# Performance work log

Measured on AMD Instinct MI355X. Metric: run time of the kernel, lower is better.

## Reference

```python
import jax, jax.numpy as jnp
import numpy as np
import math

B, S, D, H, HD, P = 2, 2048, 2048, 16, 128, 10
ROPE_BASE = 10000.0


def _rope_tables(seq_len, head_dim):
    inv_freq = 1.0 / (ROPE_BASE ** (np.arange(0, head_dim, 2, dtype=np.float32) / head_dim))
    t = np.arange(seq_len, dtype=np.float32)
    freqs = np.outer(t, inv_freq)                  # [S, hd/2]
    emb = np.concatenate([freqs, freqs], axis=-1)  # [S, hd]
    return jnp.asarray(np.cos(emb)), jnp.asarray(np.sin(emb))


def _rotate_half(x):
    half = x.shape[-1] // 2
    return jnp.concatenate([-x[..., half:], x[..., :half]], axis=-1)


def setup_inputs() -> dict:
    key = jax.random.key(0)
    ks = jax.random.split(key, 8)
    hidden_states = jax.random.normal(ks[0], (B, S, D), dtype=jnp.float32)
    # causal additive mask, llama convention: 0 where allowed, large negative above diagonal
    causal = jnp.triu(jnp.full((S, S), -1e9, dtype=jnp.float32), k=1)
    attention_mask = jnp.broadcast_to(causal[None, None], (B, 1, S, S))
    position_ids = jnp.broadcast_to(jnp.arange(S, dtype=jnp.int64)[None], (B, S))
    scale = 1.0 / math.sqrt(D)
    Wq = jax.random.normal(ks[1], (D, D), dtype=jnp.float32) * scale
    Wk = jax.random.normal(ks[2], (D, D), dtype=jnp.float32) * scale
    Wv = jax.random.normal(ks[3], (D, D), dtype=jnp.float32) * scale
    Wo = jax.random.normal(ks[4], (D, D), dtype=jnp.float32) * scale
    adapter_query = jax.random.normal(ks[5], (P, D), dtype=jnp.float32)
    adapter_gate = jax.random.normal(ks[6], (1, H, 1, 1), dtype=jnp.float32) * 0.1
    return dict(hidden_states=hidden_states, attention_mask=attention_mask,
                position_ids=position_ids, Wq=Wq, Wk=Wk, Wv=Wv, Wo=Wo,
                adapter_query=adapter_query, adapter_gate=adapter_gate)


def reference(hidden_states, attention_mask, position_ids, Wq, Wk, Wv, Wo,
              adapter_query, adapter_gate):
    bsz, q_len, _ = hidden_states.shape
    inv_sqrt_hd = 1.0 / math.sqrt(HD)

    def split_heads(x):  # [B,S,D] -> [B,H,S,hd]
        return x.reshape(bsz, q_len, H, HD).transpose(0, 2, 1, 3)

    q = split_heads(hidden_states @ Wq)
    k = split_heads(hidden_states @ Wk)
    v = split_heads(hidden_states @ Wv)

    # RoPE
    cos_t, sin_t = _rope_tables(q_len, HD)
    cos = cos_t[position_ids][:, None]  # [B,1,S,hd]
    sin = sin_t[position_ids][:, None]
    q = q * cos + _rotate_half(q) * sin
    k = k * cos + _rotate_half(k) * sin

    # main attention
    scores = jnp.einsum('bhqd,bhkd->bhqk', q, k) * inv_sqrt_hd
    scores = scores + attention_mask
    attn = jax.nn.softmax(scores.astype(jnp.float32), axis=-1).astype(q.dtype)
    attn_out = jnp.einsum('bhqk,bhkd->bhqd', attn, v)

    # adapter: soft prompt projected through k/v proj (learn_kv=False), no RoPE
    adapter = jnp.broadcast_to(adapter_query[None], (bsz, P, D))  # [B,P,D]
    a_k = (adapter @ Wk).reshape(bsz, P, H, HD).transpose(0, 2, 1, 3)  # [B,H,P,hd]
    a_v = (adapter @ Wv).reshape(bsz, P, H, HD).transpose(0, 2, 1, 3)
    a_scores = jnp.einsum('bhqd,bhpd->bhqp', q, a_k) * inv_sqrt_hd
    a_w = adapter_gate * jax.nn.softmax(a_scores.astype(jnp.float32), axis=-1).astype(q.dtype)
    a_out = jnp.einsum('bhqp,bhpd->bhqd', a_w, a_v)

    out = attn_out + a_out
    out = out.transpose(0, 2, 1, 3).reshape(bsz, q_len, D)
    return out @ Wo
```

## Files before the change

### kernel.cpp

```cpp
#include <hip/hip_runtime.h>
#include <cstdint>
#include <cstddef>

typedef __bf16 bf16x8 __attribute__((ext_vector_type(8)));
typedef float  f32x4  __attribute__((ext_vector_type(4)));

__device__ __forceinline__ unsigned short f2bf(float f) {
  unsigned int u = __float_as_uint(f);
  u += 0x7FFF + ((u >> 16) & 1);
  return (unsigned short)(u >> 16);
}
__device__ __forceinline__ float bf2f(unsigned short u) {
  return __uint_as_float(((unsigned int)u) << 16);
}

#define SEQ 2048
#define DMODEL 2048
#define NH 16
#define HD 128
#define NB 2
#define NP 10
#define MAUG 4106
#define SCALEL2 (0.08838834764831845f * 1.44269504088896340f)

#define GLOAD_LDS16(g, l) \
  __builtin_amdgcn_global_load_lds((__attribute__((address_space(1))) const void*)(g), \
                                   (__attribute__((address_space(3))) void*)(l), 16, 0, 0)

#define FENCE() asm volatile("" ::: "memory")
#define SBAR() do { FENCE(); __builtin_amdgcn_s_barrier(); FENCE(); } while (0)
#define WAITVM(N) asm volatile("s_waitcnt vmcnt(" #N ")" ::: "memory")

__global__ void k_tables(float* __restrict__ cost, float* __restrict__ sint) {
  int idx = blockIdx.x * 256 + threadIdx.x;
  if (idx >= SEQ * 64) return;
  int s = idx >> 6, i = idx & 63;
  double invf = exp(-((double)(2 * i) / 128.0) * log(10000.0));
  double a = (double)s * invf;
  float c = (float)cos(a), sn = (float)sin(a);
  cost[s * HD + i] = c;  cost[s * HD + 64 + i] = c;
  sint[s * HD + i] = sn; sint[s * HD + 64 + i] = sn;
}

__global__ __launch_bounds__(256) void k_wt(const float* __restrict__ W0,
                                            const float* __restrict__ W1,
                                            const float* __restrict__ W2,
                                            const float* __restrict__ W3,
                                            unsigned short* __restrict__ out) {
  __shared__ float tile[32][33];
  const float* W = (blockIdx.z == 0) ? W0 : (blockIdx.z == 1) ? W1 : (blockIdx.z == 2) ? W2 : W3;
  unsigned short* o = out + (size_t)blockIdx.z * DMODEL * DMODEL;
  int bx = blockIdx.x * 32, by = blockIdx.y * 32;
  int tx = threadIdx.x & 31, ty = threadIdx.x >> 5;
  #pragma unroll
  for (int j = 0; j < 32; j += 8)
    tile[ty + j][tx] = W[(size_t)(bx + ty + j) * DMODEL + by + tx];
  __syncthreads();
  #pragma unroll
  for (int j = 0; j < 32; j += 8)
    o[(size_t)(by + ty + j) * DMODEL + bx + tx] = f2bf(tile[tx][ty + j]);
}

__global__ void k_xaug(const float* __restrict__ X, const float* __restrict__ Aq,
                       unsigned short* __restrict__ xaug) {
  size_t idx = (size_t)blockIdx.x * 256 + threadIdx.x;
  if (idx >= (size_t)MAUG * DMODEL) return;
  size_t row = idx >> 11;
  int col = (int)(idx & 2047);
  float v = (row < (size_t)NB * SEQ) ? X[idx] : Aq[(row - NB * SEQ) * DMODEL + col];
  xaug[idx] = f2bf(v);
}

#define RD_A(dst, bb, MH) do { \
  _Pragma("unroll") for (int i_ = 0; i_ < 4; i_++) \
    _Pragma("unroll") for (int ks_ = 0; ks_ < 2; ks_++) \
      dst[i_][ks_] = *(const bf16x8*)&lds[(bb) + (wr*128 + (MH)*64 + i_*16 + lr)*64 + (((ks_*4+quad) ^ (lr & 7)) * 8)]; \
} while (0)

#define RD_B(dst, bb, NHH) do { \
  _Pragma("unroll") for (int j_ = 0; j_ < 2; j_++) \
    _Pragma("unroll") for (int ks_ = 0; ks_ < 2; ks_++) \
      dst[j_][ks_] = *(const bf16x8*)&lds[(bb) + 16384 + (wc*64 + (NHH)*32 + j_*16 + lr)*64 + (((ks_*4+quad) ^ (lr & 7)) * 8)]; \
} while (0)

#define MM(A, B, MH, NHH) do { \
  __builtin_amdgcn_s_setprio(1); \
  _Pragma("unroll") for (int i_ = 0; i_ < 4; i_++) \
    _Pragma("unroll") for (int j_ = 0; j_ < 2; j_++) { \
      acc[(MH)*4+i_][(NHH)*2+j_] = __builtin_amdgcn_mfma_f32_16x16x32_bf16(A[i_][0], B[j_][0], acc[(MH)*4+i_][(NHH)*2+j_], 0, 0, 0); \
      acc[(MH)*4+i_][(NHH)*2+j_] = __builtin_amdgcn_mfma_f32_16x16x32_bf16(A[i_][1], B[j_][1], acc[(MH)*4+i_][(NHH)*2+j_], 0, 0, 0); \
    } \
  __builtin_amdgcn_s_setprio(0); \
} while (0)

#define STG_AE(nb, ko) do { \
  GLOAD_LDS16(sA + (ko),                      &lds[(nb)*32768 + (qrow)*64 + g8]); \
  GLOAD_LDS16(sA + 128*(size_t)DMODEL + (ko), &lds[(nb)*32768 + (128+qrow)*64 + g8]); } while (0)
#define STG_AO(nb, ko) do { \
  GLOAD_LDS16(sA + 64*(size_t)DMODEL + (ko),  &lds[(nb)*32768 + (64+qrow)*64 + g8]); \
  GLOAD_LDS16(sA + 192*(size_t)DMODEL + (ko), &lds[(nb)*32768 + (192+qrow)*64 + g8]); } while (0)
#define STG_BE(nb, ko) do { \
  GLOAD_LDS16(sB + (ko),                      &lds[(nb)*32768 + 16384 + (qb)*64 + g8]); \
  GLOAD_LDS16(sB + 128*(size_t)DMODEL + (ko), &lds[(nb)*32768 + 16384 + (128+qb)*64 + g8]); } while (0)
#define STG_BO(nb, ko) do { \
  GLOAD_LDS16(sB + 32*(size_t)DMODEL + (ko),  &lds[(nb)*32768 + 16384 + (32+qb)*64 + g8]); \
  GLOAD_LDS16(sB + 160*(size_t)DMODEL + (ko), &lds[(nb)*32768 + 16384 + (160+qb)*64 + g8]); } while (0)

template<int BF16OUT>
__global__ __launch_bounds__(512, 2) void k_gemm256(const unsigned short* __restrict__ A,
                                                    const unsigned short* __restrict__ Bt,
                                                    void* __restrict__ Cv,
                                                    int M, size_t c_stride_mat) {
  __shared__ unsigned short lds[65536];
  const int t = threadIdx.x;
  const int lane = t & 63, w = t >> 6;
  const int lr = lane & 15, quad = lane >> 4;
  const int wr = w >> 2, wc = w & 3;
  const int tm = (M + 255) >> 8;
  const int perz = tm * 8;
  const int qchunk = gridDim.x >> 3;
  const int lin = ((int)blockIdx.x & 7) * qchunk + ((int)blockIdx.x >> 3);
  const int z = lin / perz;
  const int rem = lin - z * perz;
  const int m0 = (rem >> 3) * 256, n0 = (rem & 7) * 256;
  const unsigned short* Bz = Bt + (size_t)z * DMODEL * DMODEL;

  const int qrow = t >> 3;
  const int g8 = (t & 7) * 8;
  const int gsw8 = (((t & 7) ^ (qrow & 7)) * 8);
  const int qb = (qrow < 32) ? qrow : qrow + 32;

  const unsigned short* sA = A + (size_t)(m0 + qrow) * DMODEL + gsw8;
  const unsigned short* sB = Bz + (size_t)(n0 + qb) * DMODEL + gsw8;

  bf16x8 aE[4][2], aO[4][2], bE[2][2], bO[2][2];
  f32x4 acc[8][4];
  #pragma unroll
  for (int i = 0; i < 8; i++)
    #pragma unroll
    for (int j = 0; j < 4; j++) acc[i][j] = (f32x4){0.f, 0.f, 0.f, 0.f};

  STG_AE(0, 0); STG_BE(0, 0); STG_BO(0, 0); STG_AO(0, 0);
  WAITVM(4);
  SBAR();
  RD_A(aE, 0, 0); RD_B(bE, 0, 0);

  for (int kt = 0; kt < DMODEL / 64; kt++) {
    const int base = (kt & 1) << 15;
    const int nb2 = (kt & 1) ^ 1;
    const int nbase = nb2 << 15;
    const int ko = (kt + 1) * 64;
    const bool more = (kt + 1 < DMODEL / 64);

    if (more) { STG_AE(nb2, ko); WAITVM(4); } else WAITVM(2);
    SBAR();
    RD_B(bO, base, 1);
    MM(aE, bE, 0, 0);

    if (more) { STG_BE(nb2, ko); WAITVM(4); } else WAITVM(0);
    SBAR();
    RD_A(aO, base, 1);
    MM(aE, bO, 0, 1);

    if (more) STG_BO(nb2, ko);
    MM(aO, bE, 1, 0);

    if (more) {
      STG_AO(nb2, ko);
      WAITVM(4);
      SBAR();
      RD_A(aE, nbase, 0); RD_B(bE, nbase, 0);
    }
    MM(aO, bO, 1, 1);
  }

  #pragma unroll
  for (int mi = 0; mi < 8; mi++) {
    #pragma unroll
    for (int r = 0; r < 4; r++) {
      int row = m0 + wr * 128 + mi * 16 + quad * 4 + r;
      if (row < M) {
        if (BF16OUT) {
          unsigned short* C = (unsigned short*)Cv + (size_t)z * c_stride_mat;
          #pragma unroll
          for (int n = 0; n < 4; n++)
            C[(size_t)row * DMODEL + n0 + wc * 64 + n * 16 + lr] = f2bf(acc[mi][n][r]);
        } else {
          float* C = (float*)Cv + (size_t)z * c_stride_mat;
          #pragma unroll
          for (int n = 0; n < 4; n++)
            C[(size_t)row * DMODEL + n0 + wc * 64 + n * 16 + lr] = acc[mi][n][r];
        }
      }
    }
  }
}

#define O_LDA(MH) do { \
  _Pragma("unroll") for (int i_ = 0; i_ < 2; i_++) \
    _Pragma("unroll") for (int ks_ = 0; ks_ < 2; ks_++) \
      a[i_][ks_] = *(const bf16x8*)&lds[base + (wr*64 + ((MH)*2+i_)*16 + lr)*64 + (((ks_*4+quad) ^ (lr & 7)) * 8)]; \
} while (0)

#define O_LDB(NHH) do { \
  _Pragma("unroll") for (int j_ = 0; j_ < 2; j_++) \
    _Pragma("unroll") for (int ks_ = 0; ks_ < 2; ks_++) \
      b[(NHH)*2+j_][ks_] = *(const bf16x8*)&lds[base + 8192 + (wc*64 + ((NHH)*2+j_)*16 + lr)*64 + (((ks_*4+quad) ^ (lr & 7)) * 8)]; \
} while (0)

#define O_MFMA(MH, NHH) do { \
  __builtin_amdgcn_s_setprio(1); \
  _Pragma("unroll") for (int i_ = 0; i_ < 2; i_++) \
    _Pragma("unroll") for (int j_ = 0; j_ < 2; j_++) { \
      acc[(MH)*2+i_][(NHH)*2+j_] = __builtin_amdgcn_mfma_f32_16x16x32_bf16(a[i_][0], b[(NHH)*2+j_][0], acc[(MH)*2+i_][(NHH)*2+j_], 0, 0, 0); \
      acc[(MH)*2+i_][(NHH)*2+j_] = __builtin_amdgcn_mfma_f32_16x16x32_bf16(a[i_][1], b[(NHH)*2+j_][1], acc[(MH)*2+i_][(NHH)*2+j_], 0, 0, 0); \
    } \
  __builtin_amdgcn_s_setprio(0); \
} while (0)

#define O_STG_AE(nb, ko) GLOAD_LDS16(sA + (ko), &lds[(nb)*24576 + (qb)*64 + g8])
#define O_STG_AO(nb, ko) GLOAD_LDS16(sA + 32*(size_t)DMODEL + (ko), &lds[(nb)*24576 + (32+qb)*64 + g8])
#define O_STG_BE(nb, ko) do { \
  GLOAD_LDS16(sB + (ko),                      &lds[(nb)*24576 + 8192 + (qb)*64 + g8]); \
  GLOAD_LDS16(sB + 128*(size_t)DMODEL + (ko), &lds[(nb)*24576 + 8192 + (128+qb)*64 + g8]); } while (0)
#define O_STG_BO(nb, ko) do { \
  GLOAD_LDS16(sB + 32*(size_t)DMODEL + (ko),  &lds[(nb)*24576 + 8192 + (32+qb)*64 + g8]); \
  GLOAD_LDS16(sB + 160*(size_t)DMODEL + (ko), &lds[(nb)*24576 + 8192 + (160+qb)*64 + g8]); } while (0)

__global__ __launch_bounds__(512, 2) void k_gemmo(const unsigned short* __restrict__ A,
                                                  const unsigned short* __restrict__ Bt,
                                                  float* __restrict__ C) {
  __shared__ unsigned short lds[49152];
  const int t = threadIdx.x;
  const int lane = t & 63, w = t >> 6;
  const int lr = lane & 15, quad = lane >> 4;
  const int wr = w >> 2, wc = w & 3;
  const int lin = ((int)blockIdx.x & 7) * 32 + ((int)blockIdx.x >> 3);
  const int m0 = (lin >> 3) * 128, n0 = (lin & 7) * 256;

  const int qrow = t >> 3;
  const int g8 = (t & 7) * 8;
  const int gsw8 = (((t & 7) ^ (qrow & 7)) * 8);
  const int qb = (qrow < 32) ? qrow : qrow + 32;

  const unsigned short* sA = A + (size_t)(m0 + qb) * DMODEL + gsw8;
  const unsigned short* sB = Bt + (size_t)(n0 + qb) * DMODEL + gsw8;

  bf16x8 a[2][2], b[4][2];
  f32x4 acc[4][4];
  #pragma unroll
  for (int i = 0; i < 4; i++)
    #pragma unroll
    for (int j = 0; j < 4; j++) acc[i][j] = (f32x4){0.f, 0.f, 0.f, 0.f};

  O_STG_AE(0, 0); O_STG_BE(0, 0); O_STG_BO(0, 0); O_STG_AO(0, 0);
  WAITVM(3);
  SBAR();

  for (int kt = 0; kt < DMODEL / 64; kt++) {
    const int base = (kt & 1) * 24576;
    const int nb = (kt & 1) ^ 1;
    const int ko = (kt + 1) * 64;
    const bool more = (kt + 1 < DMODEL / 64);

    O_LDA(0);
    O_LDB(0);
    if (more) O_STG_AE(nb, ko);
    SBAR();
    O_MFMA(0, 0);
    if (more) WAITVM(2); else WAITVM(1);
    SBAR();

    O_LDB(1);
    if (more) O_STG_BE(nb, ko);
    SBAR();
    O_MFMA(0, 1);
    if (more) WAITVM(3); else WAITVM(0);
    SBAR();

    O_LDA(1);
    if (more) O_STG_BO(nb, ko);
    SBAR();
    O_MFMA(1, 0);
    SBAR();

    if (more) O_STG_AO(nb, ko);
    SBAR();
    O_MFMA(1, 1);
    if (more) WAITVM(3);
    SBAR();
  }

  #pragma unroll
  for (int mi = 0; mi < 4; mi++) {
    #pragma unroll
    for (int r = 0; r < 4; r++) {
      int row = m0 + wr * 64 + mi * 16 + quad * 4 + r;
      #pragma unroll
      for (int n = 0; n < 4; n++)
        C[(size_t)row * DMODEL + n0 + wc * 64 + n * 16 + lr] = acc[mi][n][r];
    }
  }
}

__global__ __launch_bounds__(256) void k_rope(const unsigned short* __restrict__ Qf,
                                              const unsigned short* __restrict__ Kf,
                                              const unsigned short* __restrict__ Vf,
                                              const float* __restrict__ cost, const float* __restrict__ sint,
                                              unsigned short* __restrict__ Qb, unsigned short* __restrict__ Kb,
                                              unsigned short* __restrict__ AKb, unsigned short* __restrict__ avt) {
  int row = blockIdx.x;
  int t = threadIdx.x;
  int c0 = t * 8;
  size_t off = (size_t)row * DMODEL + c0;
  if (row < NB * SEQ) {
    int s = row & (SEQ - 1);
    int d0 = c0 & (HD - 1);
    int po = (d0 < 64) ? 64 : -64;
    float sign = (d0 < 64) ? -1.f : 1.f;
    uint4 qv = *(const uint4*)&Qf[off];
    uint4 qp = *(const uint4*)&Qf[off + po];
    uint4 kv = *(const uint4*)&Kf[off];
    uint4 kp = *(const uint4*)&Kf[off + po];
    const unsigned short* qa = (const unsigned short*)&qv;
    const unsigned short* qb2 = (const unsigned short*)&qp;
    const unsigned short* ka = (const unsigned short*)&kv;
    const unsigned short* kb2 = (const unsigned short*)&kp;
    unsigned short oq[8], ok[8];
    #pragma unroll
    for (int j = 0; j < 8; j++) {
      float cv = cost[s * HD + d0 + j], sv = sint[s * HD + d0 + j];
      oq[j] = f2bf(bf2f(qa[j]) * cv + sign * bf2f(qb2[j]) * sv);
      ok[j] = f2bf(bf2f(ka[j]) * cv + sign * bf2f(kb2[j]) * sv);
    }
    *(uint4*)&Qb[off] = *(const uint4*)oq;
    *(uint4*)&Kb[off] = *(const uint4*)ok;
  } else {
    int p = row - NB * SEQ;
    uint4 kv = *(const uint4*)&Kf[off];
    uint4 vv = *(const uint4*)&Vf[off];
    *(uint4*)&AKb[(size_t)p * DMODEL + c0] = kv;
    const unsigned short* vp = (const unsigned short*)&vv;
    #pragma unroll
    for (int j = 0; j < 8; j++)
      avt[(size_t)(c0 + j) * 32 + p] = vp[j];
    if (p == 0) {
      #pragma unroll
      for (int j = 0; j < 8; j++)
        for (int pp = NP; pp < 32; pp++)
          avt[(size_t)(c0 + j) * 32 + pp] = 0;
    }
  }
}

__global__ __launch_bounds__(256) void k_vt(const unsigned short* __restrict__ Vf,
                                            unsigned short* __restrict__ Vt) {
  __shared__ unsigned short tile[64][72];
  const int t = threadIdx.x;
  int s0 = blockIdx.x * 64;
  int d0 = blockIdx.y * 64;
  int b = blockIdx.z >> 4, h = blockIdx.z & 15;
  #pragma unroll
  for (int j = t; j < 512; j += 256) {
    int row = j >> 3, ch = j & 7;
    *(uint4*)&tile[row][ch * 8] =
      *(const uint4*)&Vf[(size_t)(b * SEQ + s0 + row) * DMODEL + h * HD + d0 + ch * 8];
  }
  __syncthreads();
  #pragma unroll
  for (int j = t; j < 512; j += 256) {
    int dr = j >> 3, ch = j & 7;
    unsigned short tmp[8];
    #pragma unroll
    for (int k = 0; k < 8; k++) tmp[k] = tile[ch * 8 + k][dr];
    *(uint4*)&Vt[((size_t)((b * NH + h) * HD + d0 + dr)) * SEQ + s0 + ch * 8] = *(const uint4*)tmp;
  }
}

#define PSTR 68

__global__ __launch_bounds__(256, 2) void k_flash(const unsigned short* __restrict__ Qb,
                                               const unsigned short* __restrict__ Kb,
                                               const unsigned short* __restrict__ Vt,
                                               const unsigned short* __restrict__ AKb,
                                               const unsigned short* __restrict__ avt,
                                               const float* __restrict__ gate,
                                               unsigned short* __restrict__ Obuf,
                                               float* __restrict__ ml,
                                               unsigned short* __restrict__ Aout) {
  const int L = blockIdx.x;
  const int h = L & 15;
  const int slot = 39 - (L >> 4);
  const int b = blockIdx.y;
  int qt, j, P;
  if (slot < 4)       { qt = slot;               j = 0;          P = 1; }
  else if (slot < 12) { int s = slot - 4;  qt = 4 + (s >> 1);  j = s & 1; P = 2; }
  else if (slot < 24) { int s = slot - 12; qt = 8 + s / 3;     j = s % 3; P = 3; }
  else                { int s = slot - 24; qt = 12 + (s >> 2); j = s & 3; P = 4; }

  const int t = threadIdx.x, w = t >> 6, lane = t & 63;
  const int lr = lane & 15, quad = lane >> 4;

  __shared__ unsigned short Ks[64 * 128];
  __shared__ unsigned short Vs[128 * 64];
  __shared__ unsigned short Ps[4][32 * PSTR];
  unsigned short* Ps16 = &Ps[w][0];

  const int row_base = qt * 128 + w * 32;

  bf16x8 qf[2][4];
  #pragma unroll
  for (int mt = 0; mt < 2; mt++)
    #pragma unroll
    for (int kk = 0; kk < 4; kk++)
      qf[mt][kk] = *(const bf16x8*)&Qb[((size_t)(b * SEQ + row_base + mt * 16 + lr)) * DMODEL
                                       + h * HD + kk * 32 + quad * 8];

  f32x4 o[2][8];
  #pragma unroll
  for (int mt = 0; mt < 2; mt++)
    #pragma unroll
    for (int nt = 0; nt < 8; nt++) o[mt][nt] = (f32x4){0.f, 0.f, 0.f, 0.f};
  float l_i[2][4];
  #pragma unroll
  for (int mt = 0; mt < 2; mt++)
    #pragma unroll
    for (int r = 0; r < 4; r++) l_i[mt][r] = 0.f;

  const int krow = t >> 4;
  const int vd = t >> 3, vc = (t & 7) ^ (vd & 7);
  const int ktend = 2 * qt + 2;

  for (int kt = j; kt < ktend; kt += P) {
    __syncthreads();
    #pragma unroll
    for (int jj = 0; jj < 4; jj++) {
      int row = krow + jj * 16;
      int c = (t & 15) ^ (row & 15);
      GLOAD_LDS16(&Kb[((size_t)(b * SEQ + kt * 64 + row)) * DMODEL + h * HD + c * 8],
                  &Ks[(t + jj * 256) * 8]);
    }
    #pragma unroll
    for (int jj = 0; jj < 4; jj++) {
      int d = vd + jj * 32;
      GLOAD_LDS16(&Vt[((size_t)((b * NH + h) * HD + d)) * SEQ + kt * 64 + vc * 8],
                  &Vs[(t + jj * 256) * 8]);
    }
    __syncthreads();

    f32x4 s4[2][4];
    #pragma unroll
    for (int mt = 0; mt < 2; mt++)
      #pragma unroll
      for (int nt = 0; nt < 4; nt++) s4[mt][nt] = (f32x4){0.f, 0.f, 0.f, 0.f};
    #pragma unroll
    for (int nt = 0; nt < 4; nt++)
      #pragma unroll
      for (int kk = 0; kk < 4; kk++) {
        bf16x8 bv = *(const bf16x8*)&Ks[((nt * 16 + lr) * 16 + ((kk * 4 + quad) ^ lr)) * 8];
        s4[0][nt] = __builtin_amdgcn_mfma_f32_16x16x32_bf16(qf[0][kk], bv, s4[0][nt], 0, 0, 0);
        s4[1][nt] = __builtin_amdgcn_mfma_f32_16x16x32_bf16(qf[1][kk], bv, s4[1][nt], 0, 0, 0);
      }

    const int maybe_mask = (kt * 64 + 63 > row_base);
    #pragma unroll
    for (int mt = 0; mt < 2; mt++) {
      #pragma unroll
      for (int nt = 0; nt < 4; nt++) s4[mt][nt] = s4[mt][nt] * SCALEL2;
      if (maybe_mask) {
        #pragma unroll
        for (int nt = 0; nt < 4; nt++) {
          int col = kt * 64 + nt * 16 + lr;
          #pragma unroll
          for (int r = 0; r < 4; r++)
            if (col > row_base + mt * 16 + quad * 4 + r) s4[mt][nt][r] = -__builtin_inff();
        }
      }
      #pragma unroll
      for (int nt = 0; nt < 4; nt++)
        #pragma unroll
        for (int r = 0; r < 4; r++) {
          float p = __builtin_amdgcn_exp2f(s4[mt][nt][r]);
          l_i[mt][r] += p;
          Ps[w][(mt * 16 + quad * 4 + r) * PSTR + nt * 16 + lr] = f2bf(p);
        }
    }
    #pragma unroll
    for (int kk2 = 0; kk2 < 2; kk2++) {
      bf16x8 af0 = *(const bf16x8*)&Ps[w][(lr) * PSTR + kk2 * 32 + quad * 8];
      bf16x8 af1 = *(const bf16x8*)&Ps[w][(16 + lr) * PSTR + kk2 * 32 + quad * 8];
      #pragma unroll
      for (int nt = 0; nt < 8; nt++) {
        bf16x8 bv = *(const bf16x8*)&Vs[((nt * 16 + lr) * 8 + ((kk2 * 4 + quad) ^ (lr & 7))) * 8];
        o[0][nt] = __builtin_amdgcn_mfma_f32_16x16x32_bf16(af0, bv, o[0][nt], 0, 0, 0);
        o[1][nt] = __builtin_amdgcn_mfma_f32_16x16x32_bf16(af1, bv, o[1][nt], 0, 0, 0);
      }
    }
  }

  #pragma unroll
  for (int mt = 0; mt < 2; mt++)
    #pragma unroll
    for (int r = 0; r < 4; r++) {
      float l = l_i[mt][r];
      #pragma unroll
      for (int off = 1; off < 16; off <<= 1) l += __shfl_xor(l, off, 64);
      l_i[mt][r] = l;
    }

  const size_t slotg = (size_t)(b * 16 + h) * 40 + slot;

  if (j == 0) {
    const float g = gate[h];
    #pragma unroll
    for (int mt = 0; mt < 2; mt++) {
      f32x4 as4 = (f32x4){0.f, 0.f, 0.f, 0.f};
      #pragma unroll
      for (int kk = 0; kk < 4; kk++) {
        bf16x8 akf = *(const bf16x8*)&AKb[(size_t)lr * DMODEL + h * HD + kk * 32 + quad * 8];
        as4 = __builtin_amdgcn_mfma_f32_16x16x32_bf16(qf[mt][kk], akf, as4, 0, 0, 0);
      }
      as4 = as4 * SCALEL2;
      float al[4];
      #pragma unroll
      for (int r = 0; r < 4; r++) {
        float p = (lr < NP) ? __builtin_amdgcn_exp2f(as4[r]) : 0.f;
        as4[r] = p;
        float sum = p;
        #pragma unroll
        for (int off = 1; off < 16; off <<= 1) sum += __shfl_xor(sum, off, 64);
        al[r] = sum;
      }
      #pragma unroll
      for (int r = 0; r < 4; r++) {
        Ps[w][(mt * 16 + quad * 4 + r) * PSTR + lr] = f2bf(as4[r]);
        Ps[w][(mt * 16 + quad * 4 + r) * PSTR + 16 + lr] = 0;
      }
      bf16x8 af = *(const bf16x8*)&Ps[w][(mt * 16 + lr) * PSTR + quad * 8];
      f32x4 pa[8];
      #pragma unroll
      for (int nt = 0; nt < 8; nt++) {
        bf16x8 bv = *(const bf16x8*)&avt[(size_t)(h * HD + nt * 16 + lr) * 32 + quad * 8];
        pa[nt] = __builtin_amdgcn_mfma_f32_16x16x32_bf16(af, bv, (f32x4){0.f, 0.f, 0.f, 0.f}, 0, 0, 0);
      }
      float invla[4];
      #pragma unroll
      for (int r = 0; r < 4; r++) invla[r] = g / al[r];
      #pragma unroll
      for (int nt = 0; nt < 8; nt++)
        #pragma unroll
        for (int r = 0; r < 4; r++)
          Ps16[(quad * 4 + r) * 128 + nt * 16 + lr] = f2bf(pa[nt][r] * invla[r]);
      size_t gb = (((size_t)(b * 16 + h) * 16 + qt)) * 16384 + (size_t)(w * 32 + mt * 16) * 128;
      #pragma unroll
      for (int it = 0; it < 4; it++) {
        int i = lane + it * 64;
        int rr = i >> 4, ch = i & 15;
        *(uint4*)&Aout[gb + rr * 128 + ch * 8] = *(const uint4*)&Ps16[rr * 128 + ch * 8];
      }
    }
  }

  #pragma unroll
  for (int mt = 0; mt < 2; mt++) {
    if (lr == 0) {
      #pragma unroll
      for (int r = 0; r < 4; r++) {
        int rl = w * 32 + mt * 16 + quad * 4 + r;
        ml[slotg * 128 + rl] = l_i[mt][r];
      }
    }
    #pragma unroll
    for (int nt = 0; nt < 8; nt++)
      #pragma unroll
      for (int r = 0; r < 4; r++)
        Ps16[(quad * 4 + r) * 128 + nt * 16 + lr] = f2bf(o[mt][nt][r]);
    size_t gb = slotg * 16384 + (size_t)(w * 32 + mt * 16) * 128;
    #pragma unroll
    for (int it = 0; it < 4; it++) {
      int i = lane + it * 64;
      int rr = i >> 4, ch = i & 15;
      *(uint4*)&Obuf[gb + rr * 128 + ch * 8] = *(const uint4*)&Ps16[rr * 128 + ch * 8];
    }
  }
}

__global__ __launch_bounds__(256) void k_merge(const unsigned short* __restrict__ Obuf,
                                               const float* __restrict__ ml,
                                               const unsigned short* __restrict__ Aout,
                                               unsigned short* __restrict__ ab) {
  int idx = blockIdx.x * 256 + threadIdx.x;
  int ch = idx & 15;
  int row = (idx >> 4) & 2047;
  int h = (idx >> 15) & 15;
  int b = idx >> 19;
  int qt = row >> 7, rl = row & 127;
  int start = qt < 4 ? qt : qt < 8 ? 4 + 2 * (qt - 4) : qt < 12 ? 12 + 3 * (qt - 8) : 24 + 4 * (qt - 12);
  int P = qt < 4 ? 1 : qt < 8 ? 2 : qt < 12 ? 3 : 4;
  size_t sbase = (size_t)(b * 16 + h) * 40 + start;
  float den = 0.f;
  float acc[8] = {0.f, 0.f, 0.f, 0.f, 0.f, 0.f, 0.f, 0.f};
  #pragma unroll
  for (int jp = 0; jp < 4; jp++) {
    if (jp < P) {
      den += ml[(sbase + jp) * 128 + rl];
      uint4 ov = *(const uint4*)&Obuf[(sbase + jp) * 16384 + rl * 128 + ch * 8];
      const unsigned short* pv = (const unsigned short*)&ov;
      #pragma unroll
      for (int k = 0; k < 8; k++) acc[k] += bf2f(pv[k]);
    }
  }
  uint4 av = *(const uint4*)&Aout[(((size_t)(b * 16 + h) * 16 + qt)) * 16384 + rl * 128 + ch * 8];
  const unsigned short* pa = (const unsigned short*)&av;
  float dn = 1.0f / den;
  unsigned short res[8];
  #pragma unroll
  for (int k = 0; k < 8; k++) res[k] = f2bf(acc[k] * dn + bf2f(pa[k]));
  *(uint4*)&ab[((size_t)(b * 2048 + row)) * 2048 + h * 128 + ch * 8] = *(const uint4*)res;
}

extern "C" void kernel_launch(void* const* d_in, const int* in_sizes, int n_in,
                              void* d_out, int out_size, void* d_ws, size_t ws_size,
                              hipStream_t stream) {
  const float* hidden = (const float*)d_in[0];
  const float* Wq = (const float*)d_in[3];
  const float* Wk = (const float*)d_in[4];
  const float* Wv = (const float*)d_in[5];
  const float* Wo = (const float*)d_in[6];
  const float* Aq = (const float*)d_in[7];
  const float* gate = (const float*)d_in[8];
  float* out = (float*)d_out;

  char* ws = (char*)d_ws;
  size_t off = 0;
  auto alloc = [&](size_t bytes) -> void* {
    void* p = ws + off;
    off = (off + bytes + 255) & ~(size_t)255;
    return p;
  };
  unsigned short* wt   = (unsigned short*)alloc((size_t)4 * DMODEL * DMODEL * 2);
  unsigned short* xaug = (unsigned short*)alloc((size_t)MAUG * DMODEL * 2);
  unsigned short* qkvb = (unsigned short*)alloc((size_t)3 * MAUG * DMODEL * 2);
  unsigned short* qf = qkvb;
  unsigned short* kf = qkvb + (size_t)MAUG * DMODEL;
  unsigned short* vf = kf + (size_t)MAUG * DMODEL;
  unsigned short* qb  = (unsigned short*)alloc((size_t)NB * SEQ * DMODEL * 2);
  unsigned short* kb  = (unsigned short*)alloc((size_t)NB * SEQ * DMODEL * 2);
  unsigned short* vt  = (unsigned short*)alloc((size_t)NB * SEQ * DMODEL * 2);
  unsigned short* akb = (unsigned short*)alloc((size_t)16 * DMODEL * 2);
  unsigned short* avt = (unsigned short*)alloc((size_t)DMODEL * 32 * 2);
  float* cost = (float*)alloc((size_t)SEQ * HD * 4);
  float* sint = (float*)alloc((size_t)SEQ * HD * 4);
  unsigned short* obuf = (unsigned short*)alloc((size_t)NB * NH * 40 * 16384 * 2);
  float* mlb = (float*)alloc((size_t)NB * NH * 40 * 128 * 4);
  unsigned short* aout = (unsigned short*)alloc((size_t)NB * NH * 16 * 16384 * 2);
  unsigned short* ab = qf;

  k_tables<<<SEQ * 64 / 256, 256, 0, stream>>>(cost, sint);
  k_wt<<<dim3(64, 64, 4), 256, 0, stream>>>(Wq, Wk, Wv, Wo, wt);
  {
    size_t n = (size_t)MAUG * DMODEL;
    k_xaug<<<(unsigned)((n + 255) / 256), 256, 0, stream>>>(hidden, Aq, xaug);
  }
  k_gemm256<1><<<dim3(408), 512, 0, stream>>>(xaug, wt, qkvb, MAUG, (size_t)MAUG * DMODEL);
  k_rope<<<MAUG, 256, 0, stream>>>(qf, kf, vf, cost, sint, qb, kb, akb, avt);
  k_vt<<<dim3(32, 2, 32), 256, 0, stream>>>(vf, vt);
  k_flash<<<dim3(640, 2), 256, 0, stream>>>(qb, kb, vt, akb, avt, gate, obuf, mlb, aout);
  k_merge<<<4096, 256, 0, stream>>>(obuf, mlb, aout, ab);
  k_gemmo<<<dim3(256), 512, 0, stream>>>(ab, wt + (size_t)3 * DMODEL * DMODEL, out);
}
```

Measured before the change: 420.1 us.

## Double-buffer K tiles and prefetch next K/V during attention compute

```diff
diff --git a/kernel.cpp b/kernel.cpp
--- a/kernel.cpp
+++ b/kernel.cpp
@@ -401,7 +401,7 @@
   const int t = threadIdx.x, w = t >> 6, lane = t & 63;
   const int lr = lane & 15, quad = lane >> 4;
 
-  __shared__ unsigned short Ks[64 * 128];
+  __shared__ unsigned short Ks[2 * 64 * 128];
   __shared__ unsigned short Vs[128 * 64];
   __shared__ unsigned short Ps[4][32 * PSTR];
   unsigned short* Ps16 = &Ps[w][0];
@@ -431,22 +431,28 @@
   const int vd = t >> 3, vc = (t & 7) ^ (vd & 7);
   const int ktend = 2 * qt + 2;
 
+  #pragma unroll
+  for (int jj = 0; jj < 4; jj++) {
+    int row = krow + jj * 16;
+    int c = (t & 15) ^ (row & 15);
+    GLOAD_LDS16(&Kb[((size_t)(b * SEQ + j * 64 + row)) * DMODEL + h * HD + c * 8],
+                &Ks[(t + jj * 256) * 8]);
+  }
+  #pragma unroll
+  for (int jj = 0; jj < 4; jj++) {
+    int d = vd + jj * 32;
+    GLOAD_LDS16(&Vt[((size_t)((b * NH + h) * HD + d)) * SEQ + j * 64 + vc * 8],
+                &Vs[(t + jj * 256) * 8]);
+  }
+
+  int kb = 0;
   for (int kt = j; kt < ktend; kt += P) {
-    __syncthreads();
-    #pragma unroll
-    for (int jj = 0; jj < 4; jj++) {
-      int row = krow + jj * 16;
-      int c = (t & 15) ^ (row & 15);
-      GLOAD_LDS16(&Kb[((size_t)(b * SEQ + kt * 64 + row)) * DMODEL + h * HD + c * 8],
-                  &Ks[(t + jj * 256) * 8]);
-    }
-    #pragma unroll
-    for (int jj = 0; jj < 4; jj++) {
-      int d = vd + jj * 32;
-      GLOAD_LDS16(&Vt[((size_t)((b * NH + h) * HD + d)) * SEQ + kt * 64 + vc * 8],
-                  &Vs[(t + jj * 256) * 8]);
-    }
-    __syncthreads();
+    const bool more = (kt + P < ktend);
+    const int kbase = kb * 8192;
+    const int nkbase = 8192 - kbase;
+
+    WAITVM(4);
+    SBAR();
 
     f32x4 s4[2][4];
     #pragma unroll
@@ -457,10 +463,20 @@
     for (int nt = 0; nt < 4; nt++)
       #pragma unroll
       for (int kk = 0; kk < 4; kk++) {
-        bf16x8 bv = *(const bf16x8*)&Ks[((nt * 16 + lr) * 16 + ((kk * 4 + quad) ^ lr)) * 8];
+        bf16x8 bv = *(const bf16x8*)&Ks[kbase + ((nt * 16 + lr) * 16 + ((kk * 4 + quad) ^ lr)) * 8];
         s4[0][nt] = __builtin_amdgcn_mfma_f32_16x16x32_bf16(qf[0][kk], bv, s4[0][nt], 0, 0, 0);
         s4[1][nt] = __builtin_amdgcn_mfma_f32_16x16x32_bf16(qf[1][kk], bv, s4[1][nt], 0, 0, 0);
       }
+
+    if (more) {
+      #pragma unroll
+      for (int jj = 0; jj < 4; jj++) {
+        int row = krow + jj * 16;
+        int c = (t & 15) ^ (row & 15);
+        GLOAD_LDS16(&Kb[((size_t)(b * SEQ + (kt + P) * 64 + row)) * DMODEL + h * HD + c * 8],
+                    &Ks[nkbase + (t + jj * 256) * 8]);
+      }
+    }
 
     const int maybe_mask = (kt * 64 + 63 > row_base);
     #pragma unroll
@@ -485,6 +501,10 @@
           Ps[w][(mt * 16 + quad * 4 + r) * PSTR + nt * 16 + lr] = f2bf(p);
         }
     }
+
+    if (more) WAITVM(4); else WAITVM(0);
+    SBAR();
+
     #pragma unroll
     for (int kk2 = 0; kk2 < 2; kk2++) {
       bf16x8 af0 = *(const bf16x8*)&Ps[w][(lr) * PSTR + kk2 * 32 + quad * 8];
@@ -496,6 +516,17 @@
         o[1][nt] = __builtin_amdgcn_mfma_f32_16x16x32_bf16(af1, bv, o[1][nt], 0, 0, 0);
       }
     }
+
+    SBAR();
+    if (more) {
+      #pragma unroll
+      for (int jj = 0; jj < 4; jj++) {
+        int d = vd + jj * 32;
+        GLOAD_LDS16(&Vt[((size_t)((b * NH + h) * HD + d)) * SEQ + (kt + P) * 64 + vc * 8],
+                    &Vs[(t + jj * 256) * 8]);
+      }
+    }
+    kb ^= 1;
   }
 
   #pragma unroll
```

Result: no change. 420.7 us (+0.1%).
